# Performance work log

Measured on AMD Instinct MI355X. Metric: run time of the kernel, lower is better.

Reference implementation:

```python
import jax, jax.numpy as jnp
import numpy as np
from functools import reduce

N_QUBITS = 8
DEPTH = 2
DIM = 2 ** N_QUBITS  # state-vector dimension
HIDDEN = 512


def _cnot_chain_np(n):
    # product of CNOT(w, w+1) for w = 0..n-2, wire 0 = most-significant bit (PennyLane order)
    C4 = np.array([[1, 0, 0, 0], [0, 1, 0, 0], [0, 0, 0, 1], [0, 0, 1, 0]], dtype=np.complex64)
    U = np.eye(2 ** n, dtype=np.complex64)
    for w in range(n - 1):
        full = np.kron(np.kron(np.eye(2 ** w, dtype=np.complex64), C4),
                       np.eye(2 ** (n - w - 2), dtype=np.complex64))
        U = full @ U
    return U

CNOT_CHAIN = jnp.asarray(_cnot_chain_np(N_QUBITS))
# PauliZ on wire 0 (MSB): +1 for basis states with MSB=0, -1 otherwise
Z0 = jnp.asarray(np.where(np.arange(DIM) < DIM // 2, 1.0, -1.0).astype(np.float32))


def _rot(p):
    # PennyLane Rot(phi, theta, omega) = RZ(omega) @ RY(theta) @ RZ(phi)
    phi, th, om = p[0], p[1], p[2]
    c = jnp.cos(th / 2).astype(jnp.complex64)
    s = jnp.sin(th / 2).astype(jnp.complex64)
    ep = jnp.exp(-0.5j * (phi + om).astype(jnp.complex64))  # e^{-i(phi+om)/2}
    em = jnp.exp(0.5j * (phi - om).astype(jnp.complex64))   # e^{ i(phi-om)/2}
    m00 = ep * c
    m01 = -em * s
    m10 = jnp.conj(em) * s
    m11 = jnp.conj(ep) * c
    return jnp.stack([jnp.stack([m00, m01]), jnp.stack([m10, m11])])


def _gate_unitary(P):
    # P: (depth, n_qubits, 3). Circuit (after data RX): per layer Rot on every wire, then CNOT chain.
    U = jnp.eye(DIM, dtype=jnp.complex64)
    for l in range(DEPTH):
        layer = reduce(jnp.kron, [_rot(P[l, w]) for w in range(N_QUBITS)])
        U = CNOT_CHAIN @ (layer @ U)
    return U


def _expval(theta, U):
    # RX(theta)|0...0> = cos(t/2)|0..0> - i sin(t/2)|10..0>; then fixed unitary U; <Z_0>
    col0 = U[:, 0]          # U |00...0>
    col1 = U[:, DIM // 2]   # U |10...0>
    a = jnp.cos(theta / 2)[:, None]
    b = jnp.sin(theta / 2)[:, None]
    psi = a * col0[None, :] - 1j * b * col1[None, :]  # (B, DIM)
    return jnp.sum(Z0 * (psi.real ** 2 + psi.imag ** 2), axis=-1)  # (B,)


def setup_inputs() -> dict:
    key = jax.random.key(0)
    ks = jax.random.split(key, 13)
    T, B, D, H, Q = 256, 128, 512, HIDDEN, N_QUBITS
    inp = {"inputs": jax.random.normal(ks[0], (T, B, D), jnp.float32)}
    for i, g in enumerate(["f", "i", "g", "o"]):
        inp[f"W{g}"] = jax.random.normal(ks[1 + 3 * i], (Q, D + H), jnp.float32) * 0.02
        inp[f"b{g}"] = jnp.zeros((Q,), jnp.float32)
        inp[f"P{g}"] = jax.random.normal(ks[3 + 3 * i], (DEPTH, Q, 3), jnp.float32)
    return inp


def reference(inputs, Wf, bf, Pf, Wi, bi, Pi, Wg, bg, Pg, Wo, bo, Po):
    Uf, Ui, Ug, Uo = _gate_unitary(Pf), _gate_unitary(Pi), _gate_unitary(Pg), _gate_unitary(Po)

    def step(carry, x):
        hx, cx = carry
        comb = jnp.concatenate([x, hx], axis=1)  # (B, D+H)
        f = jax.nn.sigmoid(_expval((comb @ Wf.T + bf)[:, 0], Uf))[:, None]
        i = jax.nn.sigmoid(_expval((comb @ Wi.T + bi)[:, 0], Ui))[:, None]
        g = jnp.tanh(_expval((comb @ Wg.T + bg)[:, 0], Ug))[:, None]
        o = jax.nn.sigmoid(_expval((comb @ Wo.T + bo)[:, 0], Uo))[:, None]
        cx = f * cx + i * g
        hx = o * jnp.tanh(cx)
        return (hx, cx), hx

    B = inputs.shape[1]
    init = (jnp.zeros((B, HIDDEN), inputs.dtype), jnp.zeros((B, HIDDEN), inputs.dtype))
    (hx, cx), outputs = jax.lax.scan(step, init, inputs)
    return outputs, hx, cx
```

## Files before the change

kernel.cpp:

```cpp
#include <hip/hip_runtime.h>
#include <math.h>

#define T_STEPS 256
#define BATCH   128
#define DIMD    512
#define NROWS   (T_STEPS * BATCH)
#define PF      16
#define WRITER_BLOCKS 258
#define GEMV_BLOCKS 2048

#define INV2PI  0.15915494309189535f
#define L2E     1.4426950408889634f
#define TWO_L2E 2.8853900817779268f

#define AGENT __HIP_MEMORY_SCOPE_AGENT

typedef float f32x4 __attribute__((ext_vector_type(4)));

#if __has_builtin(__builtin_amdgcn_sinf)
#define HW_SIN(x) __builtin_amdgcn_sinf(x)
#else
__device__ __forceinline__ float HW_SIN(float x) { return __sinf(x * 6.283185307179586f); }
#endif
#if __has_builtin(__builtin_amdgcn_exp2f)
#define EXP2(x) __builtin_amdgcn_exp2f(x)
#else
#define EXP2(x) exp2f(x)
#endif
#if __has_builtin(__builtin_amdgcn_rcpf)
#define RCP(x) __builtin_amdgcn_rcpf(x)
#else
#define RCP(x) (1.0f / (x))
#endif

__device__ __forceinline__ void  st_rlx(float* p, float v) {
    __hip_atomic_store(p, v, __ATOMIC_RELAXED, AGENT);
}
__device__ __forceinline__ void  st_rlx_i(int* p, int v) {
    __hip_atomic_store(p, v, __ATOMIC_RELAXED, AGENT);
}
__device__ __forceinline__ int   ld_rlx_i(const int* p) {
    return __hip_atomic_load(p, __ATOMIC_RELAXED, AGENT);
}
#define VMFENCE() asm volatile("s_waitcnt vmcnt(0)" ::: "memory")
#define CFENCE()  asm volatile("" ::: "memory")

__global__ __launch_bounds__(256) void prep(
    const float* __restrict__ inp,
    const float* __restrict__ Wf, const float* __restrict__ Wi,
    const float* __restrict__ Wg, const float* __restrict__ Wo,
    const float* __restrict__ bfp, const float* __restrict__ bip,
    const float* __restrict__ bgp, const float* __restrict__ bop,
    const float* __restrict__ Pf, const float* __restrict__ Pi,
    const float* __restrict__ Pg, const float* __restrict__ Po,
    float* __restrict__ gc, int* __restrict__ hProg,
    float4* __restrict__ X4)
{
    const int bid  = blockIdx.x;
    const int wv   = threadIdx.x >> 6;
    const int lane = threadIdx.x & 63;

    if (bid == 0) {
        if (threadIdx.x == 0) { hProg[0] = 0; hProg[1] = 0; }
        const int g = wv;
        const float* P = (g == 0) ? Pf : (g == 1) ? Pi : (g == 2) ? Pg : Po;
        const float* W = (g == 0) ? Wf : (g == 1) ? Wi : (g == 2) ? Wg : Wo;

        __shared__ float s0r[4][256], s0i[4][256], s1r[4][256], s1i[4][256];

#pragma unroll
        for (int j = 0; j < 4; ++j) {
            const int k = lane + 64 * j;
            s0r[g][k] = (k == 0)   ? 1.0f : 0.0f;  s0i[g][k] = 0.0f;
            s1r[g][k] = (k == 128) ? 1.0f : 0.0f;  s1i[g][k] = 0.0f;
        }
        __syncthreads();

        for (int l = 0; l < 2; ++l) {
            for (int w = 0; w < 8; ++w) {
                const float phi = P[l * 24 + w * 3 + 0];
                const float th  = P[l * 24 + w * 3 + 1];
                const float om  = P[l * 24 + w * 3 + 2];
                float sh, chh; __sincosf(0.5f * th, &sh, &chh);
                float sp, cp;  __sincosf(0.5f * (phi + om), &sp, &cp);
                float sm, cm;  __sincosf(0.5f * (phi - om), &sm, &cm);
                const float m00r =  cp * chh, m00i = -sp * chh;
                const float m01r = -cm * sh,  m01i = -sm * sh;
                const float m10r =  cm * sh,  m10i = -sm * sh;
                const float m11r =  cp * chh, m11i =  sp * chh;

                const int shift = 7 - w;
                const int mask  = 1 << shift;

                float n0r[4], n0i[4], n1r[4], n1i[4];
#pragma unroll
                for (int j = 0; j < 4; ++j) {
                    const int k  = lane + 64 * j;
                    const int bit = (k >> shift) & 1;
                    const int i0 = k & ~mask, i1 = k | mask;
                    const float a0r = s0r[g][i0], a0i = s0i[g][i0];
                    const float a1r = s0r[g][i1], a1i = s0i[g][i1];
                    const float b0r = s1r[g][i0], b0i = s1i[g][i0];
                    const float b1r = s1r[g][i1], b1i = s1i[g][i1];
                    const float mr0 = bit ? m10r : m00r, mi0 = bit ? m10i : m00i;
                    const float mr1 = bit ? m11r : m01r, mi1 = bit ? m11i : m01i;
                    n0r[j] = mr0 * a0r - mi0 * a0i + mr1 * a1r - mi1 * a1i;
                    n0i[j] = mr0 * a0i + mi0 * a0r + mr1 * a1i + mi1 * a1r;
                    n1r[j] = mr0 * b0r - mi0 * b0i + mr1 * b1r - mi1 * b1i;
                    n1i[j] = mr0 * b0i + mi0 * b0r + mr1 * b1i + mi1 * b1r;
                }
                __syncthreads();
#pragma unroll
                for (int j = 0; j < 4; ++j) {
                    const int k = lane + 64 * j;
                    s0r[g][k] = n0r[j]; s0i[g][k] = n0i[j];
                    s1r[g][k] = n1r[j]; s1i[g][k] = n1i[j];
                }
                __syncthreads();
            }
            float n0r[4], n0i[4], n1r[4], n1i[4];
#pragma unroll
            for (int j = 0; j < 4; ++j) {
                int src = lane + 64 * j;
                for (int w = 6; w >= 0; --w) {
                    const int cb = (src >> (7 - w)) & 1;
                    src ^= cb << (6 - w);
                }
                n0r[j] = s0r[g][src]; n0i[j] = s0i[g][src];
                n1r[j] = s1r[g][src]; n1i[j] = s1i[g][src];
            }
            __syncthreads();
#pragma unroll
            for (int j = 0; j < 4; ++j) {
                const int k = lane + 64 * j;
                s0r[g][k] = n0r[j]; s0i[g][k] = n0i[j];
                s1r[g][k] = n1r[j]; s1i[g][k] = n1i[j];
            }
            __syncthreads();
        }

        float t00 = 0, t11 = 0, t01 = 0;
#pragma unroll
        for (int j = 0; j < 4; ++j) {
            const int k = lane + 64 * j;
            const float z = (k < 128) ? 1.0f : -1.0f;
            t00 += z * (s0r[g][k] * s0r[g][k] + s0i[g][k] * s0i[g][k]);
            t11 += z * (s1r[g][k] * s1r[g][k] + s1i[g][k] * s1i[g][k]);
            t01 += z * (s0i[g][k] * s1r[g][k] - s0r[g][k] * s1i[g][k]);
        }
        float tsw = 0;
#pragma unroll
        for (int j = 0; j < 8; ++j) tsw += W[512 + lane + 64 * j];

        for (int off = 32; off; off >>= 1) {
            t00 += __shfl_xor(t00, off);
            t11 += __shfl_xor(t11, off);
            t01 += __shfl_xor(t01, off);
            tsw += __shfl_xor(tsw, off);
        }
        if (lane == 0) {
            const float A  = 0.5f * (t00 + t11);
            const float Bc = 0.5f * (t00 - t11);
            const float Bs = -t01;
            const float R  = sqrtf(Bc * Bc + Bs * Bs);
            const float ph = atan2f(Bc, Bs) * INV2PI;
            const float sc = (g == 2) ? TWO_L2E : -L2E;
            gc[4 * g + 0] = sc * A;
            gc[4 * g + 1] = sc * R;
            gc[4 * g + 2] = ph;
            gc[4 * g + 3] = tsw * INV2PI;
        }
        return;
    }

    const int rowbase = (bid - 1) * 16 + wv * 4;

    const float4* wfp = (const float4*)Wf;
    const float4* wip = (const float4*)Wi;
    const float4* wgp = (const float4*)Wg;
    const float4* wop = (const float4*)Wo;
    const float4 fa = wfp[lane], fb = wfp[lane + 64];
    const float4 ia = wip[lane], ib = wip[lane + 64];
    const float4 ga = wgp[lane], gb = wgp[lane + 64];
    const float4 oa = wop[lane], ob = wop[lane + 64];

    const float4* xr = (const float4*)(inp + (size_t)rowbase * DIMD);
    float sums[4][4];
#pragma unroll
    for (int r = 0; r < 4; ++r) {
        const float4 xa = xr[r * 128 + lane];
        const float4 xb = xr[r * 128 + lane + 64];
        sums[r][0] = xa.x * fa.x + xa.y * fa.y + xa.z * fa.z + xa.w * fa.w
                   + xb.x * fb.x + xb.y * fb.y + xb.z * fb.z + xb.w * fb.w;
        sums[r][1] = xa.x * ia.x + xa.y * ia.y + xa.z * ia.z + xa.w * ia.w
                   + xb.x * ib.x + xb.y * ib.y + xb.z * ib.z + xb.w * ib.w;
        sums[r][2] = xa.x * ga.x + xa.y * ga.y + xa.z * ga.z + xa.w * ga.w
                   + xb.x * gb.x + xb.y * gb.y + xb.z * gb.z + xb.w * gb.w;
        sums[r][3] = xa.x * oa.x + xa.y * oa.y + xa.z * oa.z + xa.w * oa.w
                   + xb.x * ob.x + xb.y * ob.y + xb.z * ob.z + xb.w * ob.w;
    }
#pragma unroll
    for (int r = 0; r < 4; ++r)
#pragma unroll
        for (int g = 0; g < 4; ++g)
            for (int off = 32; off; off >>= 1)
                sums[r][g] += __shfl_xor(sums[r][g], off);

    if (lane == 0) {
        const float b0f = bfp[0], b0i = bip[0], b0g = bgp[0], b0o = bop[0];
#pragma unroll
        for (int r = 0; r < 4; ++r) {
            X4[rowbase + r] = make_float4((sums[r][0] + b0f) * INV2PI,
                                          (sums[r][1] + b0i) * INV2PI,
                                          (sums[r][2] + b0g) * INV2PI,
                                          (sums[r][3] + b0o) * INV2PI);
        }
    }
}

__global__ __launch_bounds__(256) void scan_write(
    const float4* __restrict__ X4, const float* __restrict__ gc,
    float* __restrict__ Hs, float* __restrict__ cfin,
    float4* __restrict__ out4, int* __restrict__ hProg)
{
    const int bid  = blockIdx.x;
    const int wv   = threadIdx.x >> 6;
    const int lane = threadIdx.x & 63;

    if (bid == 0) {
        if (threadIdx.x >= BATCH) return;
        const int b = threadIdx.x;

        const float Af = gc[0],  Rf = gc[1],  phf = gc[2],  swf = gc[3];
        const float Ai = gc[4],  Ri = gc[5],  phi_ = gc[6], swi = gc[7];
        const float Ag = gc[8],  Rg = gc[9],  phg = gc[10], swg = gc[11];
        const float Ao = gc[12], Ro = gc[13], pho = gc[14], swo = gc[15];

        float4 p[PF], q[PF];
#pragma unroll
        for (int j = 0; j < PF; ++j) {
            const float4 v = X4[j * BATCH + b];
            p[j] = make_float4(v.x + phf, v.y + phi_, v.z + phg, v.w + pho);
        }

        float c = 0.0f, h = 0.0f;
        for (int k = 0; k < T_STEPS / PF; ++k) {
            const int tb = k * PF;
#pragma unroll
            for (int j = 0; j < PF; ++j) q[j] = X4[(tb + PF + j) * BATCH + b];
#pragma unroll
            for (int j = 0; j < PF; ++j) {
                const float4 xv = p[j];
                const float thf = fmaf(h, swf, xv.x);
                const float thi = fmaf(h, swi, xv.y);
                const float thg = fmaf(h, swg, xv.z);
                const float tho = fmaf(h, swo, xv.w);
                const float ef = EXP2(fmaf(Rf, HW_SIN(thf), Af));
                const float ei = EXP2(fmaf(Ri, HW_SIN(thi), Ai));
                const float eg = EXP2(fmaf(Rg, HW_SIN(thg), Ag));
                const float eo = EXP2(fmaf(Ro, HW_SIN(tho), Ao));
                const float Ff = ef + 1.0f, Fi = ei + 1.0f;
                const float Fg = eg + 1.0f, Fo = eo + 1.0f;
                const float FiFg = Fi * Fg;
                const float num  = fmaf(c, FiFg, (eg - 1.0f) * Ff);
                c = num * RCP(Ff * FiFg);
                const float ec = EXP2(c * TWO_L2E);
                h = (ec - 1.0f) * RCP(Fo * (ec + 1.0f));
                st_rlx(&Hs[(tb + j) * BATCH + b], h);
            }
            if (k == T_STEPS / PF - 1) st_rlx(&cfin[b], c);
            if ((k & 3) == 3) {
                VMFENCE();
                if (lane == 0) st_rlx_i(&hProg[wv], tb + PF);
            }
#pragma unroll
            for (int j = 0; j < PF; ++j) {
                p[j] = make_float4(q[j].x + phf, q[j].y + phi_,
                                   q[j].z + phg, q[j].w + pho);
            }
        }
        return;
    }

    const int t  = bid - 1;
    const int qd = wv;
    const int pidx = (qd < 2) ? 0 : 1;
    const int need = (t < 256) ? ((t >> 6) + 1) << 6 : 256;

    int cur = ld_rlx_i(&hProg[pidx]);
    while (cur < need) {
        int loops = ((need - cur) >> 5) + 1;
        for (int s = 0; s < loops; ++s) {
            __builtin_amdgcn_s_sleep(32);
            __builtin_amdgcn_s_sleep(32);
        }
        cur = ld_rlx_i(&hProg[pidx]);
    }
    CFENCE();

    const float* src = (t == 257) ? cfin : (Hs + ((t >= 256 ? 255 : t) * BATCH));
    const float hv = src[qd * 32 + (lane & 31)];

    size_t base = (t < 256) ? ((size_t)t * 16384)
                : (t == 256 ? (size_t)4194304 : (size_t)4210688);
    base += (size_t)qd * 4096;
#pragma unroll 8
    for (int j = 0; j < 64; ++j) {
        const float v = __shfl(hv, j >> 1);
        const f32x4 val = {v, v, v, v};
        __builtin_nontemporal_store(val, (f32x4*)(out4 + base + j * 64 + lane));
    }
}

extern "C" void kernel_launch(void* const* d_in, const int* in_sizes, int n_in,
                              void* d_out, int out_size, void* d_ws, size_t ws_size,
                              hipStream_t stream)
{
    const float* inp = (const float*)d_in[0];
    const float* Wf  = (const float*)d_in[1];
    const float* bfv = (const float*)d_in[2];
    const float* Pf  = (const float*)d_in[3];
    const float* Wi  = (const float*)d_in[4];
    const float* biv = (const float*)d_in[5];
    const float* Pi  = (const float*)d_in[6];
    const float* Wg  = (const float*)d_in[7];
    const float* bgv = (const float*)d_in[8];
    const float* Pg  = (const float*)d_in[9];
    const float* Wo  = (const float*)d_in[10];
    const float* bov = (const float*)d_in[11];
    const float* Po  = (const float*)d_in[12];

    float4* X4   = (float4*)d_ws;
    float*  Hs   = (float*)(X4 + NROWS + PF * BATCH);
    float*  cfin = Hs + NROWS;
    float*  gc   = cfin + BATCH;
    int*    hProg = (int*)(gc + 16);

    prep<<<1 + GEMV_BLOCKS, 256, 0, stream>>>(inp, Wf, Wi, Wg, Wo,
                                              bfv, biv, bgv, bov,
                                              Pf, Pi, Pg, Po,
                                              gc, hProg, X4);
    scan_write<<<1 + WRITER_BLOCKS, 256, 0, stream>>>(X4, gc, Hs, cfin,
                                                      (float4*)d_out, hProg);
}
```

Before: 55.19 us.

## Split scan block into producer and compute waves with LDS double-buffering

The serial scan block now uses two waves as producers. They prefetch the next chunk of precomputed gate inputs from global memory into a double-buffered LDS array. The other two waves run the recurrence, reading inputs from LDS instead of holding a register prefetch array. Chunks are synchronised with __syncthreads, and a single progress counter is published after the barrier, which replaces the per-wave vmcnt fence. This is meant to cut register pressure and global-load latency on the critical serial path, at the cost of a block barrier on every chunk.

```diff
diff --git a/kernel.cpp b/kernel.cpp
--- a/kernel.cpp
+++ b/kernel.cpp
@@ -6,6 +6,7 @@
 #define DIMD    512
 #define NROWS   (T_STEPS * BATCH)
 #define PF      16
+#define NCHUNK  (T_STEPS / PF)
 #define WRITER_BLOCKS 258
 #define GEMV_BLOCKS 2048
 
@@ -42,7 +43,6 @@
 __device__ __forceinline__ int   ld_rlx_i(const int* p) {
     return __hip_atomic_load(p, __ATOMIC_RELAXED, AGENT);
 }
-#define VMFENCE() asm volatile("s_waitcnt vmcnt(0)" ::: "memory")
 #define CFENCE()  asm volatile("" ::: "memory")
 
 __global__ __launch_bounds__(256) void prep(
@@ -224,77 +224,90 @@
     float4* __restrict__ out4, int* __restrict__ hProg)
 {
     const int bid  = blockIdx.x;
-    const int wv   = threadIdx.x >> 6;
-    const int lane = threadIdx.x & 63;
+    const int tid  = threadIdx.x;
+    const int wv   = tid >> 6;
+    const int lane = tid & 63;
 
     if (bid == 0) {
-        if (threadIdx.x >= BATCH) return;
-        const int b = threadIdx.x;
-
-        const float Af = gc[0],  Rf = gc[1],  phf = gc[2],  swf = gc[3];
-        const float Ai = gc[4],  Ri = gc[5],  phi_ = gc[6], swi = gc[7];
-        const float Ag = gc[8],  Rg = gc[9],  phg = gc[10], swg = gc[11];
-        const float Ao = gc[12], Ro = gc[13], pho = gc[14], swo = gc[15];
-
-        float4 p[PF], q[PF];
-#pragma unroll
-        for (int j = 0; j < PF; ++j) {
-            const float4 v = X4[j * BATCH + b];
-            p[j] = make_float4(v.x + phf, v.y + phi_, v.z + phg, v.w + pho);
-        }
+        __shared__ float4 xbuf[2][PF][BATCH];
+
+        const float phf = gc[2], phi_ = gc[6], phg = gc[10], pho = gc[14];
+
+        if (tid >= BATCH) {
+            const int b = tid - BATCH;
+#pragma unroll
+            for (int j = 0; j < PF; ++j) {
+                const float4 v = X4[j * BATCH + b];
+                xbuf[0][j][b] = make_float4(v.x + phf, v.y + phi_,
+                                            v.z + phg, v.w + pho);
+            }
+        }
+        __syncthreads();
+
+        const float Af = gc[0],  Rf = gc[1],  swf = gc[3];
+        const float Ai = gc[4],  Ri = gc[5],  swi = gc[7];
+        const float Ag = gc[8],  Rg = gc[9],  swg = gc[11];
+        const float Ao = gc[12], Ro = gc[13], swo = gc[15];
 
         float c = 0.0f, h = 0.0f;
-        for (int k = 0; k < T_STEPS / PF; ++k) {
+        for (int k = 0; k < NCHUNK; ++k) {
             const int tb = k * PF;
-#pragma unroll
-            for (int j = 0; j < PF; ++j) q[j] = X4[(tb + PF + j) * BATCH + b];
-#pragma unroll
-            for (int j = 0; j < PF; ++j) {
-                const float4 xv = p[j];
-                const float thf = fmaf(h, swf, xv.x);
-                const float thi = fmaf(h, swi, xv.y);
-                const float thg = fmaf(h, swg, xv.z);
-                const float tho = fmaf(h, swo, xv.w);
-                const float ef = EXP2(fmaf(Rf, HW_SIN(thf), Af));
-                const float ei = EXP2(fmaf(Ri, HW_SIN(thi), Ai));
-                const float eg = EXP2(fmaf(Rg, HW_SIN(thg), Ag));
-                const float eo = EXP2(fmaf(Ro, HW_SIN(tho), Ao));
-                const float Ff = ef + 1.0f, Fi = ei + 1.0f;
-                const float Fg = eg + 1.0f, Fo = eo + 1.0f;
-                const float FiFg = Fi * Fg;
-                const float num  = fmaf(c, FiFg, (eg - 1.0f) * Ff);
-                c = num * RCP(Ff * FiFg);
-                const float ec = EXP2(c * TWO_L2E);
-                h = (ec - 1.0f) * RCP(Fo * (ec + 1.0f));
-                st_rlx(&Hs[(tb + j) * BATCH + b], h);
-            }
-            if (k == T_STEPS / PF - 1) st_rlx(&cfin[b], c);
-            if ((k & 3) == 3) {
-                VMFENCE();
-                if (lane == 0) st_rlx_i(&hProg[wv], tb + PF);
-            }
-#pragma unroll
-            for (int j = 0; j < PF; ++j) {
-                p[j] = make_float4(q[j].x + phf, q[j].y + phi_,
-                                   q[j].z + phg, q[j].w + pho);
-            }
+            if (tid >= BATCH) {
+                const int b  = tid - BATCH;
+                const int nb = (k + 1) & 1;
+#pragma unroll
+                for (int j = 0; j < PF; ++j) {
+                    const float4 v = X4[(tb + PF + j) * BATCH + b];
+                    xbuf[nb][j][b] = make_float4(v.x + phf, v.y + phi_,
+                                                 v.z + phg, v.w + pho);
+                }
+            } else {
+                const int b  = tid;
+                const int cb = k & 1;
+                float4 xv = xbuf[cb][0][b];
+#pragma unroll
+                for (int j = 0; j < PF; ++j) {
+                    float4 nx;
+                    if (j < PF - 1) nx = xbuf[cb][j + 1][b];
+                    const float thf = fmaf(h, swf, xv.x);
+                    const float thi = fmaf(h, swi, xv.y);
+                    const float thg = fmaf(h, swg, xv.z);
+                    const float tho = fmaf(h, swo, xv.w);
+                    const float ef = EXP2(fmaf(Rf, HW_SIN(thf), Af));
+                    const float ei = EXP2(fmaf(Ri, HW_SIN(thi), Ai));
+                    const float eg = EXP2(fmaf(Rg, HW_SIN(thg), Ag));
+                    const float eo = EXP2(fmaf(Ro, HW_SIN(tho), Ao));
+                    const float Ff = ef + 1.0f, Fi = ei + 1.0f;
+                    const float Fg = eg + 1.0f, Fo = eo + 1.0f;
+                    const float FiFg = Fi * Fg;
+                    const float num  = fmaf(c, FiFg, (eg - 1.0f) * Ff);
+                    c = num * RCP(Ff * FiFg);
+                    const float ec = EXP2(c * TWO_L2E);
+                    h = (ec - 1.0f) * RCP(Fo * (ec + 1.0f));
+                    st_rlx(&Hs[(tb + j) * BATCH + b], h);
+                    xv = nx;
+                }
+                if (k == NCHUNK - 1) st_rlx(&cfin[b], c);
+            }
+            __syncthreads();
+            if ((k & 3) == 3 && tid == 0)
+                st_rlx_i(&hProg[0], tb + PF);
         }
         return;
     }
 
     const int t  = bid - 1;
     const int qd = wv;
-    const int pidx = (qd < 2) ? 0 : 1;
     const int need = (t < 256) ? ((t >> 6) + 1) << 6 : 256;
 
-    int cur = ld_rlx_i(&hProg[pidx]);
+    int cur = ld_rlx_i(&hProg[0]);
     while (cur < need) {
         int loops = ((need - cur) >> 5) + 1;
         for (int s = 0; s < loops; ++s) {
             __builtin_amdgcn_s_sleep(32);
             __builtin_amdgcn_s_sleep(32);
         }
-        cur = ld_rlx_i(&hProg[pidx]);
+        cur = ld_rlx_i(&hProg[0]);
     }
     CFENCE();
 
```

After: 54.87 us. About the same (-0.6%).
